# Performance work log

Hardware: AMD Instinct MI355X
Metric: run time of the kernel (lower is better)

## Reference

```python
import jax, jax.numpy as jnp
import numpy as np

N_NODES = 100_000
N_EDGES = 20_000   # hyperedges
NNZ = 2_000_000    # incidence pairs
F = 128
BN_EPS = 1e-5


def setup_inputs() -> dict:
    key = jax.random.key(0)
    ks = jax.random.split(key, 6)
    x_0 = jax.random.normal(ks[0], (N_NODES, F), dtype=jnp.float32)
    x_1 = jax.random.normal(ks[1], (N_EDGES, F), dtype=jnp.float32)
    node_idx = jax.random.randint(ks[2], (NNZ,), 0, N_NODES, dtype=jnp.int32)
    edge_idx = jax.random.randint(ks[3], (NNZ,), 0, N_EDGES, dtype=jnp.int32)
    W_nh = jax.random.normal(ks[4], (F, F), dtype=jnp.float32) / np.float32(np.sqrt(F))
    b_nh = jnp.zeros((F,), jnp.float32)
    W_en = jax.random.normal(ks[5], (F, 2 * F), dtype=jnp.float32) / np.float32(np.sqrt(2 * F))
    b_en = jnp.zeros((F,), jnp.float32)
    ones = jnp.ones((F,), jnp.float32)
    zeros = jnp.zeros((F,), jnp.float32)
    return {
        "x_0": x_0, "x_1": x_1, "node_idx": node_idx, "edge_idx": edge_idx,
        "W_nh": W_nh, "b_nh": b_nh, "W_en": W_en, "b_en": b_en,
        "bn0_gamma": ones, "bn0_beta": zeros, "bn0_mean": zeros, "bn0_var": ones,
        "bn1_gamma": ones, "bn1_beta": zeros, "bn1_mean": zeros, "bn1_var": ones,
    }


def _bn_eval(x, gamma, beta, mean, var):
    # BatchNorm1d in eval mode: normalize with running stats.
    return (x - mean) * (gamma * jax.lax.rsqrt(var + BN_EPS)) + beta


def reference(x_0, x_1, node_idx, edge_idx, W_nh, b_nh, W_en, b_en,
              bn0_gamma, bn0_beta, bn0_mean, bn0_var,
              bn1_gamma, bn1_beta, bn1_mean, bn1_var):
    # --- node -> hyperedge messenger ---
    # per-node message: sigmoid(Linear(x_0))  [n_nodes, F]
    node_messages = jax.nn.sigmoid(x_0 @ W_nh.T + b_nh)
    # gather over incidence list, scatter-sum onto hyperedges  [n_edges, F]
    node_msg_agg = jax.ops.segment_sum(node_messages[node_idx], edge_idx,
                                       num_segments=N_EDGES)

    # --- hyperedge -> node messenger ---
    # per-hyperedge message: sigmoid(Linear(cat(x_1, agg node msgs)))  [n_edges, F]
    he_messages = jax.nn.sigmoid(
        jnp.concatenate([x_1, node_msg_agg], axis=1) @ W_en.T + b_en)
    # gather per incidence, scatter-sum onto nodes  [n_nodes, F]
    he_msg_agg = jax.ops.segment_sum(he_messages[edge_idx], node_idx,
                                     num_segments=N_NODES)

    # --- updates (eval mode: feature dropout is identity) ---
    x0_out = jax.nn.sigmoid(
        _bn_eval(x_0, bn0_gamma, bn0_beta, bn0_mean, bn0_var) + he_msg_agg)
    x1_out = jax.nn.sigmoid(
        _bn_eval(x_1, bn1_gamma, bn1_beta, bn1_mean, bn1_var) + node_msg_agg)
    return (x0_out, x1_out)
```

## Files before the change

kernel.cpp:

```cpp
#include <hip/hip_runtime.h>
#include <hip/hip_bf16.h>
#include <math.h>

#define NNODES 100000
#define NEDGES 20000
#define NNZ_   2000000
#define FDIM   128
#define BN_EPS 1e-5f

#define NBUCK 256
#define CAP   9216
#define BPB_E 79
#define BPB_N 391
#define SH_E  17
#define SH_N  15

typedef __attribute__((ext_vector_type(8))) short bf16x8_t;
typedef __attribute__((ext_vector_type(4))) float f32x4_t;
typedef __attribute__((ext_vector_type(8))) unsigned short u16x8_t;

__device__ __forceinline__ float sigmoidf_(float x) {
    return 1.0f / (1.0f + __expf(-x));
}
__device__ __forceinline__ float bf2f(unsigned short u) {
    return __uint_as_float(((unsigned)u) << 16);
}
__device__ __forceinline__ unsigned short f2bf(float f) {
    __hip_bfloat16 h = __float2bfloat16(f);
    return *reinterpret_cast<unsigned short*>(&h);
}

__global__ __launch_bounds__(256) void prep_w(
    const float* __restrict__ W_nh, const float* __restrict__ W_en,
    unsigned short* __restrict__ Wnh_bf,
    unsigned short* __restrict__ W1hi, unsigned short* __restrict__ W1lo,
    unsigned short* __restrict__ W2hi, unsigned short* __restrict__ W2lo)
{
    int idx = blockIdx.x * blockDim.x + threadIdx.x;
    if (idx < FDIM * FDIM) {
        Wnh_bf[idx] = f2bf(W_nh[idx]);
        return;
    }
    int j = idx - FDIM * FDIM;
    if (j >= 2 * FDIM * FDIM) return;
    int n = j >> 8, kk = j & 255;
    float w = W_en[n * 2 * FDIM + kk];
    unsigned short hi = f2bf(w);
    unsigned short lo = f2bf(w - bf2f(hi));
    int o = n * FDIM + (kk & 127);
    if (kk < FDIM) { W1hi[o] = hi; W1lo[o] = lo; }
    else           { W2hi[o] = hi; W2lo[o] = lo; }
}

__global__ __launch_bounds__(256) void gemm1_mfma(
    const float* __restrict__ x0, const unsigned short* __restrict__ Wb,
    const float* __restrict__ bias, unsigned short* __restrict__ out)
{
    __shared__ unsigned short As[32][FDIM + 8];
    const int tid  = threadIdx.x;
    const int row0 = blockIdx.x * 32;
    {
        int r = tid >> 3, c0 = (tid & 7) * 16;
        const float* src = x0 + (size_t)(row0 + r) * FDIM + c0;
        unsigned short* dst = &As[r][c0];
        #pragma unroll
        for (int i = 0; i < 4; i++) {
            float4 v = *(const float4*)(src + i * 4);
            dst[i * 4 + 0] = f2bf(v.x);
            dst[i * 4 + 1] = f2bf(v.y);
            dst[i * 4 + 2] = f2bf(v.z);
            dst[i * 4 + 3] = f2bf(v.w);
        }
    }
    __syncthreads();
    const int wave  = tid >> 6;
    const int lane  = tid & 63;
    const int mhalf = wave & 1;
    const int nhalf = wave >> 1;
    const int lm    = lane & 15;
    const int quad  = lane >> 4;
    f32x4_t acc[4] = {};
    #pragma unroll
    for (int ks = 0; ks < 4; ks++) {
        bf16x8_t a = *(const bf16x8_t*)&As[mhalf * 16 + lm][ks * 32 + quad * 8];
        #pragma unroll
        for (int nt = 0; nt < 4; nt++) {
            int n = nhalf * 64 + nt * 16 + lm;
            bf16x8_t b = *(const bf16x8_t*)(Wb + (size_t)n * FDIM + ks * 32 + quad * 8);
            acc[nt] = __builtin_amdgcn_mfma_f32_16x16x32_bf16(a, b, acc[nt], 0, 0, 0);
        }
    }
    const int mbase = row0 + mhalf * 16 + quad * 4;
    #pragma unroll
    for (int nt = 0; nt < 4; nt++) {
        int n = nhalf * 64 + nt * 16 + lm;
        float bv = bias[n];
        #pragma unroll
        for (int r2 = 0; r2 < 4; r2++) {
            out[(size_t)(mbase + r2) * FDIM + n] = f2bf(sigmoidf_(acc[nt][r2] + bv));
        }
    }
}

__global__ __launch_bounds__(256) void gemm2_mfma(
    const float* __restrict__ x1, const float* __restrict__ Bagg,
    const unsigned short* __restrict__ W1hi, const unsigned short* __restrict__ W1lo,
    const unsigned short* __restrict__ W2hi, const unsigned short* __restrict__ W2lo,
    const float* __restrict__ bias, unsigned short* __restrict__ out)
{
    __shared__ unsigned short Ax[2][32][FDIM + 8];
    __shared__ unsigned short Ab[2][32][FDIM + 8];
    const int tid  = threadIdx.x;
    const int row0 = blockIdx.x * 32;
    {
        int r = tid >> 3, c0 = (tid & 7) * 16;
        const float* sx = x1   + (size_t)(row0 + r) * FDIM + c0;
        const float* sb = Bagg + (size_t)(row0 + r) * FDIM + c0;
        #pragma unroll
        for (int i = 0; i < 4; i++) {
            float4 v = *(const float4*)(sx + i * 4);
            float4 w = *(const float4*)(sb + i * 4);
            #pragma unroll
            for (int c = 0; c < 4; c++) {
                float fv = (c == 0) ? v.x : (c == 1) ? v.y : (c == 2) ? v.z : v.w;
                unsigned short h = f2bf(fv);
                Ax[0][r][c0 + i * 4 + c] = h;
                Ax[1][r][c0 + i * 4 + c] = f2bf(fv - bf2f(h));
                float fw = (c == 0) ? w.x : (c == 1) ? w.y : (c == 2) ? w.z : w.w;
                unsigned short hb = f2bf(fw);
                Ab[0][r][c0 + i * 4 + c] = hb;
                Ab[1][r][c0 + i * 4 + c] = f2bf(fw - bf2f(hb));
            }
        }
    }
    __syncthreads();
    const int wave  = tid >> 6;
    const int lane  = tid & 63;
    const int mhalf = wave & 1;
    const int nhalf = wave >> 1;
    const int lm    = lane & 15;
    const int quad  = lane >> 4;
    f32x4_t acc[4] = {};
    const unsigned short* Wsel[6] = {W1hi, W1hi, W1lo, W2hi, W2hi, W2lo};
    #pragma unroll
    for (int ps = 0; ps < 6; ps++) {
        const unsigned short (*Asel)[FDIM + 8] =
            (ps < 3) ? ((ps == 1) ? Ax[1] : Ax[0])
                     : ((ps == 4) ? Ab[1] : Ab[0]);
        const unsigned short* Wp = Wsel[ps];
        #pragma unroll
        for (int ks = 0; ks < 4; ks++) {
            bf16x8_t a = *(const bf16x8_t*)&Asel[mhalf * 16 + lm][ks * 32 + quad * 8];
            #pragma unroll
            for (int nt = 0; nt < 4; nt++) {
                int n = nhalf * 64 + nt * 16 + lm;
                bf16x8_t b = *(const bf16x8_t*)(Wp + (size_t)n * FDIM + ks * 32 + quad * 8);
                acc[nt] = __builtin_amdgcn_mfma_f32_16x16x32_bf16(a, b, acc[nt], 0, 0, 0);
            }
        }
    }
    const int mbase = row0 + mhalf * 16 + quad * 4;
    #pragma unroll
    for (int nt = 0; nt < 4; nt++) {
        int n = nhalf * 64 + nt * 16 + lm;
        float bv = bias[n];
        #pragma unroll
        for (int r2 = 0; r2 < 4; r2++) {
            out[(size_t)(mbase + r2) * FDIM + n] = f2bf(sigmoidf_(acc[nt][r2] + bv));
        }
    }
}

__global__ __launch_bounds__(1024) void bucket_scatter(
    const int* __restrict__ ni, const int* __restrict__ ei,
    unsigned* __restrict__ buck_e, unsigned* __restrict__ buck_n,
    int* __restrict__ gcur_e, int* __restrict__ gcur_n)
{
    __shared__ int lh_e[NBUCK], lh_n[NBUCK], lb_e[NBUCK], lb_n[NBUCK];
    const int t = threadIdx.x;
    if (t < NBUCK) { lh_e[t] = 0; lh_n[t] = 0; }
    __syncthreads();
    unsigned ent_e[4], ent_n[4];
    int be[4], bn[4], re[4], rn[4];
    const int base = blockIdx.x * 4096;
    #pragma unroll
    for (int j = 0; j < 4; j++) {
        int i = base + j * 1024 + t;
        if (i < NNZ_) {
            unsigned n = (unsigned)ni[i], e = (unsigned)ei[i];
            ent_e[j] = (e << SH_E) | n;  be[j] = (int)(e / BPB_E);
            ent_n[j] = (n << SH_N) | e;  bn[j] = (int)(n / BPB_N);
            re[j] = atomicAdd(&lh_e[be[j]], 1);
            rn[j] = atomicAdd(&lh_n[bn[j]], 1);
        } else { be[j] = -1; }
    }
    __syncthreads();
    if (t < NBUCK) {
        lb_e[t] = t * CAP + atomicAdd(&gcur_e[t], lh_e[t]);
        lb_n[t] = t * CAP + atomicAdd(&gcur_n[t], lh_n[t]);
    }
    __syncthreads();
    #pragma unroll
    for (int j = 0; j < 4; j++) {
        if (be[j] >= 0) {
            buck_e[(size_t)lb_e[be[j]] + re[j]] = ent_e[j];
            buck_n[(size_t)lb_n[bn[j]] + rn[j]] = ent_n[j];
        }
    }
}

template<int BPB, int SH, unsigned MASK, int NBINS, typename OUT>
__device__ __forceinline__ void sort_bucket(
    const unsigned* __restrict__ region, int cnt, int gbase, int b0,
    OUT* __restrict__ csr, int* __restrict__ off)
{
    __shared__ unsigned lh[512];
    __shared__ unsigned lw[4];
    const int t = threadIdx.x;
    lh[t] = 0; lh[t + 256] = 0;
    __syncthreads();
    for (int i = t; i < cnt; i += 256) {
        int bin = (int)(region[i] >> SH) - b0;
        atomicAdd(&lh[bin], 1u);
    }
    __syncthreads();
    unsigned h0 = lh[2 * t], h1 = lh[2 * t + 1];
    unsigned s = h0 + h1, inc = s;
    const int lane = t & 63;
    #pragma unroll
    for (int d = 1; d <= 32; d <<= 1) {
        unsigned v = (unsigned)__shfl_up((int)inc, d, 64);
        if (lane >= d) inc += v;
    }
    if (lane == 63) lw[t >> 6] = inc;
    __syncthreads();
    unsigned pre = 0;
    #pragma unroll
    for (int w = 0; w < 4; w++) if (w < (t >> 6)) pre += lw[w];
    unsigned excl = pre + inc - s;
    unsigned c0 = (unsigned)gbase + excl;
    unsigned c1 = c0 + h0;
    lh[2 * t] = c0; lh[2 * t + 1] = c1;
    int i0 = 2 * t, i1 = 2 * t + 1;
    if (i0 <= BPB && b0 + i0 <= NBINS) off[b0 + i0] = (int)c0;
    if (i1 <= BPB && b0 + i1 <= NBINS) off[b0 + i1] = (int)c1;
    __syncthreads();
    for (int i = t; i < cnt; i += 256) {
        unsigned ent = region[i];
        int bin = (int)(ent >> SH) - b0;
        unsigned pos = atomicAdd(&lh[bin], 1u);
        csr[pos] = (OUT)(ent & MASK);
    }
}

__global__ __launch_bounds__(256) void bucket_sort(
    const unsigned* __restrict__ buck_e, const unsigned* __restrict__ buck_n,
    const int* __restrict__ gcur_e, const int* __restrict__ gcur_n,
    unsigned* __restrict__ csr_e, unsigned short* __restrict__ csr_n,
    int* __restrict__ off_e, int* __restrict__ off_n)
{
    const int b = blockIdx.x & 255;
    const int* gc = (blockIdx.x < 256) ? gcur_e : gcur_n;
    __shared__ int ws4[4];
    const int t = threadIdx.x;
    int v = (t < b) ? gc[t] : 0;
    #pragma unroll
    for (int d = 32; d > 0; d >>= 1) v += __shfl_down(v, d, 64);
    if ((t & 63) == 0) ws4[t >> 6] = v;
    __syncthreads();
    const int gbase = ws4[0] + ws4[1] + ws4[2] + ws4[3];
    const int cnt = gc[b];
    __syncthreads();
    if (blockIdx.x < 256)
        sort_bucket<BPB_E, SH_E, 0x1FFFFu, NEDGES, unsigned>(
            buck_e + (size_t)b * CAP, cnt, gbase, b * BPB_E, csr_e, off_e);
    else
        sort_bucket<BPB_N, SH_N, 0x7FFFu, NNODES, unsigned short>(
            buck_n + (size_t)b * CAP, cnt, gbase, b * BPB_N, csr_n, off_n);
}

template<typename IDX, int U>
__global__ __launch_bounds__(256) void seg_sum_fin_v2(
    const unsigned short* __restrict__ table, const IDX* __restrict__ csr,
    const int* __restrict__ off, const float* __restrict__ x,
    const float* __restrict__ g, const float* __restrict__ bb,
    const float* __restrict__ mm, const float* __restrict__ vv,
    float* __restrict__ agg_out, float* __restrict__ fin_out, int nseg)
{
    const int seg = blockIdx.x * 4 + (threadIdx.x >> 6);
    if (seg >= nseg) return;
    const int lane = threadIdx.x & 63;
    const int c    = lane & 15;
    const int sub  = lane >> 4;
    const int c8   = c * 8;

    const int i0 = off[seg], i1 = off[seg + 1];
    f32x4_t a0 = {}, a1 = {};

    int i = i0;
    for (; i + 4 * U <= i1; i += 4 * U) {
        int r[U];
        u16x8_t v[U];
        #pragma unroll
        for (int u = 0; u < U; u++) r[u] = (int)csr[i + 4 * u + sub];
        #pragma unroll
        for (int u = 0; u < U; u++)
            v[u] = *(const u16x8_t*)(table + (size_t)r[u] * FDIM + c8);
        #pragma unroll
        for (int u = 0; u < U; u++) {
            a0[0] += bf2f(v[u][0]); a0[1] += bf2f(v[u][1]);
            a0[2] += bf2f(v[u][2]); a0[3] += bf2f(v[u][3]);
            a1[0] += bf2f(v[u][4]); a1[1] += bf2f(v[u][5]);
            a1[2] += bf2f(v[u][6]); a1[3] += bf2f(v[u][7]);
        }
    }
    if (i < i1) {
        u16x8_t v[U];
        #pragma unroll
        for (int u = 0; u < U; u++) {
            int row = i + 4 * u + sub;
            u16x8_t z = {};
            v[u] = z;
            if (row < i1)
                v[u] = *(const u16x8_t*)(table + (size_t)csr[row] * FDIM + c8);
        }
        #pragma unroll
        for (int u = 0; u < U; u++) {
            a0[0] += bf2f(v[u][0]); a0[1] += bf2f(v[u][1]);
            a0[2] += bf2f(v[u][2]); a0[3] += bf2f(v[u][3]);
            a1[0] += bf2f(v[u][4]); a1[1] += bf2f(v[u][5]);
            a1[2] += bf2f(v[u][6]); a1[3] += bf2f(v[u][7]);
        }
    }

    #pragma unroll
    for (int j = 0; j < 4; j++) {
        a0[j] += __shfl_xor(a0[j], 16, 64);
        a0[j] += __shfl_xor(a0[j], 32, 64);
        a1[j] += __shfl_xor(a1[j], 16, 64);
        a1[j] += __shfl_xor(a1[j], 32, 64);
    }

    if (sub < 2) {
        const int q = c8 + sub * 4;
        f32x4_t s = sub ? a1 : a0;
        if (agg_out)
            *(f32x4_t*)(agg_out + (size_t)seg * FDIM + q) = s;
        if (fin_out) {
            f32x4_t xv = *(const f32x4_t*)(x + (size_t)seg * FDIM + q);
            f32x4_t gg = *(const f32x4_t*)(g + q);
            f32x4_t bt = *(const f32x4_t*)(bb + q);
            f32x4_t mn = *(const f32x4_t*)(mm + q);
            f32x4_t vr = *(const f32x4_t*)(vv + q);
            f32x4_t o;
            #pragma unroll
            for (int j = 0; j < 4; j++)
                o[j] = sigmoidf_((xv[j] - mn[j]) * (gg[j] * rsqrtf(vr[j] + BN_EPS))
                                 + bt[j] + s[j]);
            *(f32x4_t*)(fin_out + (size_t)seg * FDIM + q) = o;
        }
    }
}

extern "C" void kernel_launch(void* const* d_in, const int* in_sizes, int n_in,
                              void* d_out, int out_size, void* d_ws, size_t ws_size,
                              hipStream_t stream)
{
    const float* x0       = (const float*)d_in[0];
    const float* x1       = (const float*)d_in[1];
    const int*   node_idx = (const int*)d_in[2];
    const int*   edge_idx = (const int*)d_in[3];
    const float* W_nh     = (const float*)d_in[4];
    const float* b_nh     = (const float*)d_in[5];
    const float* W_en     = (const float*)d_in[6];
    const float* b_en     = (const float*)d_in[7];
    const float* bn0g = (const float*)d_in[8];
    const float* bn0b = (const float*)d_in[9];
    const float* bn0m = (const float*)d_in[10];
    const float* bn0v = (const float*)d_in[11];
    const float* bn1g = (const float*)d_in[12];
    const float* bn1b = (const float*)d_in[13];
    const float* bn1m = (const float*)d_in[14];
    const float* bn1v = (const float*)d_in[15];

    float* ws = (float*)d_ws;
    float* B = ws;
    unsigned short* Wnh_bf = (unsigned short*)(B + (size_t)NEDGES * FDIM);
    unsigned short* W1hi = Wnh_bf + FDIM * FDIM;
    unsigned short* W1lo = W1hi + FDIM * FDIM;
    unsigned short* W2hi = W1lo + FDIM * FDIM;
    unsigned short* W2lo = W2hi + FDIM * FDIM;
    unsigned short* A_bf = W2lo + FDIM * FDIM;
    unsigned short* D_bf = A_bf + (size_t)NNODES * FDIM;
    int* off_e = (int*)(D_bf + (size_t)NEDGES * FDIM);
    int* off_n = off_e + 20004;
    unsigned* csr_e = (unsigned*)(off_n + 100004);
    unsigned short* csr_n = (unsigned short*)(csr_e + NNZ_);
    unsigned* buck_e = (unsigned*)(csr_n + NNZ_);
    unsigned* buck_n = buck_e + (size_t)NBUCK * CAP;
    int* gcur_e = (int*)(buck_n + (size_t)NBUCK * CAP);
    int* gcur_n = gcur_e + NBUCK;

    hipMemsetAsync(gcur_e, 0, 2 * NBUCK * sizeof(int), stream);
    bucket_scatter<<<(NNZ_ + 4095) / 4096, 1024, 0, stream>>>(
        node_idx, edge_idx, buck_e, buck_n, gcur_e, gcur_n);
    bucket_sort<<<2 * NBUCK, 256, 0, stream>>>(buck_e, buck_n, gcur_e, gcur_n,
                                               csr_e, csr_n, off_e, off_n);

    prep_w<<<(3 * FDIM * FDIM + 255) / 256, 256, 0, stream>>>(
        W_nh, W_en, Wnh_bf, W1hi, W1lo, W2hi, W2lo);

    float* out0 = (float*)d_out;
    float* out1 = out0 + (size_t)NNODES * FDIM;

    gemm1_mfma<<<NNODES / 32, 256, 0, stream>>>(x0, Wnh_bf, b_nh, A_bf);
    seg_sum_fin_v2<unsigned, 8><<<(NEDGES + 3) / 4, 256, 0, stream>>>(
        A_bf, csr_e, off_e, x1, bn1g, bn1b, bn1m, bn1v, B, out1, NEDGES);

    gemm2_mfma<<<NEDGES / 32, 256, 0, stream>>>(
        x1, B, W1hi, W1lo, W2hi, W2lo, b_en, D_bf);
    seg_sum_fin_v2<unsigned short, 4><<<(NNODES + 3) / 4, 256, 0, stream>>>(
        D_bf, csr_n, off_n, x0, bn0g, bn0b, bn0m, bn0v, nullptr, out0, NNODES);
}
```

Baseline: 384.9 us.

## Fuse bucket scatter with GEMM1, fold memset into prep, register-based GEMM2

Bucket scatter and the node GEMM now run as one launch: the leading blocks do the scatter and the rest run GEMM1 tiles. GEMM1 tiles load and convert A fragments straight into registers instead of staging them in shared memory. The gcur counters are zeroed inside prep_w, which replaces the separate memset and moves prep_w ahead of the fused kernel. GEMM2 also drops shared-memory staging, building hi/lo bf16 split fragments in registers and splitting columns across two blocks per row tile for more parallelism. This cuts launch count and LDS traffic, at the cost of redundant global loads and conversions of A across waves.

Result: slower. 393.8 us (+2.3%).

```diff
diff --git a/kernel.cpp b/kernel.cpp
--- a/kernel.cpp
+++ b/kernel.cpp
@@ -34,9 +34,11 @@
     const float* __restrict__ W_nh, const float* __restrict__ W_en,
     unsigned short* __restrict__ Wnh_bf,
     unsigned short* __restrict__ W1hi, unsigned short* __restrict__ W1lo,
-    unsigned short* __restrict__ W2hi, unsigned short* __restrict__ W2lo)
+    unsigned short* __restrict__ W2hi, unsigned short* __restrict__ W2lo,
+    int* __restrict__ gcur)
 {
     int idx = blockIdx.x * blockDim.x + threadIdx.x;
+    if (idx < 2 * NBUCK) gcur[idx] = 0;
     if (idx < FDIM * FDIM) {
         Wnh_bf[idx] = f2bf(W_nh[idx]);
         return;
@@ -52,41 +54,33 @@
     else           { W2hi[o] = hi; W2lo[o] = lo; }
 }
 
-__global__ __launch_bounds__(256) void gemm1_mfma(
+__device__ __forceinline__ void gemm1_tile(
     const float* __restrict__ x0, const unsigned short* __restrict__ Wb,
-    const float* __restrict__ bias, unsigned short* __restrict__ out)
-{
-    __shared__ unsigned short As[32][FDIM + 8];
-    const int tid  = threadIdx.x;
-    const int row0 = blockIdx.x * 32;
-    {
-        int r = tid >> 3, c0 = (tid & 7) * 16;
-        const float* src = x0 + (size_t)(row0 + r) * FDIM + c0;
-        unsigned short* dst = &As[r][c0];
-        #pragma unroll
-        for (int i = 0; i < 4; i++) {
-            float4 v = *(const float4*)(src + i * 4);
-            dst[i * 4 + 0] = f2bf(v.x);
-            dst[i * 4 + 1] = f2bf(v.y);
-            dst[i * 4 + 2] = f2bf(v.z);
-            dst[i * 4 + 3] = f2bf(v.w);
-        }
-    }
-    __syncthreads();
+    const float* __restrict__ bias, unsigned short* __restrict__ out,
+    int row0, int tid)
+{
     const int wave  = tid >> 6;
     const int lane  = tid & 63;
     const int mhalf = wave & 1;
     const int nhalf = wave >> 1;
     const int lm    = lane & 15;
     const int quad  = lane >> 4;
+    const float* ar = x0 + (size_t)(row0 + mhalf * 16 + lm) * FDIM;
     f32x4_t acc[4] = {};
     #pragma unroll
     for (int ks = 0; ks < 4; ks++) {
-        bf16x8_t a = *(const bf16x8_t*)&As[mhalf * 16 + lm][ks * 32 + quad * 8];
+        const int ko = ks * 32 + quad * 8;
+        float4 f0 = *(const float4*)(ar + ko);
+        float4 f1 = *(const float4*)(ar + ko + 4);
+        bf16x8_t a;
+        a[0] = (short)f2bf(f0.x); a[1] = (short)f2bf(f0.y);
+        a[2] = (short)f2bf(f0.z); a[3] = (short)f2bf(f0.w);
+        a[4] = (short)f2bf(f1.x); a[5] = (short)f2bf(f1.y);
+        a[6] = (short)f2bf(f1.z); a[7] = (short)f2bf(f1.w);
         #pragma unroll
         for (int nt = 0; nt < 4; nt++) {
             int n = nhalf * 64 + nt * 16 + lm;
-            bf16x8_t b = *(const bf16x8_t*)(Wb + (size_t)n * FDIM + ks * 32 + quad * 8);
+            bf16x8_t b = *(const bf16x8_t*)(Wb + (size_t)n * FDIM + ko);
             acc[nt] = __builtin_amdgcn_mfma_f32_16x16x32_bf16(a, b, acc[nt], 0, 0, 0);
         }
     }
@@ -102,109 +96,126 @@
     }
 }
 
-__global__ __launch_bounds__(256) void gemm2_mfma(
+__global__ __launch_bounds__(1024) void scatter_gemm1(
+    const int* __restrict__ ni, const int* __restrict__ ei,
+    unsigned* __restrict__ buck_e, unsigned* __restrict__ buck_n,
+    int* __restrict__ gcur_e, int* __restrict__ gcur_n,
+    const float* __restrict__ x0, const unsigned short* __restrict__ Wb,
+    const float* __restrict__ bias, unsigned short* __restrict__ A_bf,
+    int nscatter)
+{
+    if (blockIdx.x < nscatter) {
+        __shared__ int lh_e[NBUCK], lh_n[NBUCK], lb_e[NBUCK], lb_n[NBUCK];
+        const int t = threadIdx.x;
+        if (t < NBUCK) { lh_e[t] = 0; lh_n[t] = 0; }
+        __syncthreads();
+        unsigned ent_e[4], ent_n[4];
+        int be[4], bn[4], re[4], rn[4];
+        const int base = blockIdx.x * 4096;
+        #pragma unroll
+        for (int j = 0; j < 4; j++) {
+            int i = base + j * 1024 + t;
+            if (i < NNZ_) {
+                unsigned n = (unsigned)ni[i], e = (unsigned)ei[i];
+                ent_e[j] = (e << SH_E) | n;  be[j] = (int)(e / BPB_E);
+                ent_n[j] = (n << SH_N) | e;  bn[j] = (int)(n / BPB_N);
+                re[j] = atomicAdd(&lh_e[be[j]], 1);
+                rn[j] = atomicAdd(&lh_n[bn[j]], 1);
+            } else { be[j] = -1; }
+        }
+        __syncthreads();
+        if (t < NBUCK) {
+            lb_e[t] = t * CAP + atomicAdd(&gcur_e[t], lh_e[t]);
+            lb_n[t] = t * CAP + atomicAdd(&gcur_n[t], lh_n[t]);
+        }
+        __syncthreads();
+        #pragma unroll
+        for (int j = 0; j < 4; j++) {
+            if (be[j] >= 0) {
+                buck_e[(size_t)lb_e[be[j]] + re[j]] = ent_e[j];
+                buck_n[(size_t)lb_n[bn[j]] + rn[j]] = ent_n[j];
+            }
+        }
+    } else {
+        const int bid  = blockIdx.x - nscatter;
+        const int row0 = bid * 128 + (threadIdx.x >> 8) * 32;
+        if (row0 >= NNODES) return;
+        gemm1_tile(x0, Wb, bias, A_bf, row0, threadIdx.x & 255);
+    }
+}
+
+__device__ __forceinline__ void mfma_pass2(
+    const bf16x8_t af[4], const unsigned short* __restrict__ W,
+    int ncol, int lm, int quad, f32x4_t acc[2])
+{
+    #pragma unroll
+    for (int ks = 0; ks < 4; ks++) {
+        #pragma unroll
+        for (int nt = 0; nt < 2; nt++) {
+            int n = ncol + nt * 16 + lm;
+            bf16x8_t b = *(const bf16x8_t*)(W + (size_t)n * FDIM + ks * 32 + quad * 8);
+            acc[nt] = __builtin_amdgcn_mfma_f32_16x16x32_bf16(af[ks], b, acc[nt], 0, 0, 0);
+        }
+    }
+}
+
+__global__ __launch_bounds__(256) void gemm2_reg(
     const float* __restrict__ x1, const float* __restrict__ Bagg,
     const unsigned short* __restrict__ W1hi, const unsigned short* __restrict__ W1lo,
     const unsigned short* __restrict__ W2hi, const unsigned short* __restrict__ W2lo,
     const float* __restrict__ bias, unsigned short* __restrict__ out)
 {
-    __shared__ unsigned short Ax[2][32][FDIM + 8];
-    __shared__ unsigned short Ab[2][32][FDIM + 8];
+    const int row0 = (blockIdx.x >> 1) * 32;
+    const int col0 = (blockIdx.x & 1) * 64;
     const int tid  = threadIdx.x;
-    const int row0 = blockIdx.x * 32;
-    {
-        int r = tid >> 3, c0 = (tid & 7) * 16;
-        const float* sx = x1   + (size_t)(row0 + r) * FDIM + c0;
-        const float* sb = Bagg + (size_t)(row0 + r) * FDIM + c0;
-        #pragma unroll
-        for (int i = 0; i < 4; i++) {
-            float4 v = *(const float4*)(sx + i * 4);
-            float4 w = *(const float4*)(sb + i * 4);
-            #pragma unroll
-            for (int c = 0; c < 4; c++) {
-                float fv = (c == 0) ? v.x : (c == 1) ? v.y : (c == 2) ? v.z : v.w;
-                unsigned short h = f2bf(fv);
-                Ax[0][r][c0 + i * 4 + c] = h;
-                Ax[1][r][c0 + i * 4 + c] = f2bf(fv - bf2f(h));
-                float fw = (c == 0) ? w.x : (c == 1) ? w.y : (c == 2) ? w.z : w.w;
-                unsigned short hb = f2bf(fw);
-                Ab[0][r][c0 + i * 4 + c] = hb;
-                Ab[1][r][c0 + i * 4 + c] = f2bf(fw - bf2f(hb));
-            }
-        }
-    }
-    __syncthreads();
     const int wave  = tid >> 6;
     const int lane  = tid & 63;
     const int mhalf = wave & 1;
-    const int nhalf = wave >> 1;
+    const int npair = wave >> 1;
     const int lm    = lane & 15;
     const int quad  = lane >> 4;
-    f32x4_t acc[4] = {};
-    const unsigned short* Wsel[6] = {W1hi, W1hi, W1lo, W2hi, W2hi, W2lo};
-    #pragma unroll
-    for (int ps = 0; ps < 6; ps++) {
-        const unsigned short (*Asel)[FDIM + 8] =
-            (ps < 3) ? ((ps == 1) ? Ax[1] : Ax[0])
-                     : ((ps == 4) ? Ab[1] : Ab[0]);
-        const unsigned short* Wp = Wsel[ps];
-        #pragma unroll
-        for (int ks = 0; ks < 4; ks++) {
-            bf16x8_t a = *(const bf16x8_t*)&Asel[mhalf * 16 + lm][ks * 32 + quad * 8];
-            #pragma unroll
-            for (int nt = 0; nt < 4; nt++) {
-                int n = nhalf * 64 + nt * 16 + lm;
-                bf16x8_t b = *(const bf16x8_t*)(Wp + (size_t)n * FDIM + ks * 32 + quad * 8);
-                acc[nt] = __builtin_amdgcn_mfma_f32_16x16x32_bf16(a, b, acc[nt], 0, 0, 0);
-            }
-        }
-    }
+    const int rowA  = row0 + mhalf * 16 + lm;
+    const float* xr = x1   + (size_t)rowA * FDIM;
+    const float* br = Bagg + (size_t)rowA * FDIM;
+
+    bf16x8_t axh[4], axl[4], abh[4], abl[4];
+    #pragma unroll
+    for (int ks = 0; ks < 4; ks++) {
+        const int ko = ks * 32 + quad * 8;
+        float4 f0 = *(const float4*)(xr + ko);
+        float4 f1 = *(const float4*)(xr + ko + 4);
+        float4 g0 = *(const float4*)(br + ko);
+        float4 g1 = *(const float4*)(br + ko + 4);
+        float fx[8] = {f0.x, f0.y, f0.z, f0.w, f1.x, f1.y, f1.z, f1.w};
+        float fb[8] = {g0.x, g0.y, g0.z, g0.w, g1.x, g1.y, g1.z, g1.w};
+        #pragma unroll
+        for (int j = 0; j < 8; j++) {
+            unsigned short h = f2bf(fx[j]);
+            axh[ks][j] = (short)h;
+            axl[ks][j] = (short)f2bf(fx[j] - bf2f(h));
+            unsigned short hb = f2bf(fb[j]);
+            abh[ks][j] = (short)hb;
+            abl[ks][j] = (short)f2bf(fb[j] - bf2f(hb));
+        }
+    }
+
+    f32x4_t acc[2] = {};
+    const int ncol = col0 + npair * 32;
+    mfma_pass2(axh, W1hi, ncol, lm, quad, acc);
+    mfma_pass2(axl, W1hi, ncol, lm, quad, acc);
+    mfma_pass2(axh, W1lo, ncol, lm, quad, acc);
+    mfma_pass2(abh, W2hi, ncol, lm, quad, acc);
+    mfma_pass2(abl, W2hi, ncol, lm, quad, acc);
+    mfma_pass2(abh, W2lo, ncol, lm, quad, acc);
+
     const int mbase = row0 + mhalf * 16 + quad * 4;
     #pragma unroll
-    for (int nt = 0; nt < 4; nt++) {
-        int n = nhalf * 64 + nt * 16 + lm;
+    for (int nt = 0; nt < 2; nt++) {
+        int n = ncol + nt * 16 + lm;
         float bv = bias[n];
         #pragma unroll
         for (int r2 = 0; r2 < 4; r2++) {
             out[(size_t)(mbase + r2) * FDIM + n] = f2bf(sigmoidf_(acc[nt][r2] + bv));
-        }
-    }
-}
-
-__global__ __launch_bounds__(1024) void bucket_scatter(
-    const int* __restrict__ ni, const int* __restrict__ ei,
-    unsigned* __restrict__ buck_e, unsigned* __restrict__ buck_n,
-    int* __restrict__ gcur_e, int* __restrict__ gcur_n)
-{
-    __shared__ int lh_e[NBUCK], lh_n[NBUCK], lb_e[NBUCK], lb_n[NBUCK];
-    const int t = threadIdx.x;
-    if (t < NBUCK) { lh_e[t] = 0; lh_n[t] = 0; }
-    __syncthreads();
-    unsigned ent_e[4], ent_n[4];
-    int be[4], bn[4], re[4], rn[4];
-    const int base = blockIdx.x * 4096;
-    #pragma unroll
-    for (int j = 0; j < 4; j++) {
-        int i = base + j * 1024 + t;
-        if (i < NNZ_) {
-            unsigned n = (unsigned)ni[i], e = (unsigned)ei[i];
-            ent_e[j] = (e << SH_E) | n;  be[j] = (int)(e / BPB_E);
-            ent_n[j] = (n << SH_N) | e;  bn[j] = (int)(n / BPB_N);
-            re[j] = atomicAdd(&lh_e[be[j]], 1);
-            rn[j] = atomicAdd(&lh_n[bn[j]], 1);
-        } else { be[j] = -1; }
-    }
-    __syncthreads();
-    if (t < NBUCK) {
-        lb_e[t] = t * CAP + atomicAdd(&gcur_e[t], lh_e[t]);
-        lb_n[t] = t * CAP + atomicAdd(&gcur_n[t], lh_n[t]);
-    }
-    __syncthreads();
-    #pragma unroll
-    for (int j = 0; j < 4; j++) {
-        if (be[j] >= 0) {
-            buck_e[(size_t)lb_e[be[j]] + re[j]] = ent_e[j];
-            buck_n[(size_t)lb_n[bn[j]] + rn[j]] = ent_n[j];
         }
     }
 }
@@ -401,24 +412,27 @@
     int* gcur_e = (int*)(buck_n + (size_t)NBUCK * CAP);
     int* gcur_n = gcur_e + NBUCK;
 
-    hipMemsetAsync(gcur_e, 0, 2 * NBUCK * sizeof(int), stream);
-    bucket_scatter<<<(NNZ_ + 4095) / 4096, 1024, 0, stream>>>(
-        node_idx, edge_idx, buck_e, buck_n, gcur_e, gcur_n);
+    prep_w<<<(3 * FDIM * FDIM + 255) / 256, 256, 0, stream>>>(
+        W_nh, W_en, Wnh_bf, W1hi, W1lo, W2hi, W2lo, gcur_e);
+
+    float* out0 = (float*)d_out;
+    float* out1 = out0 + (size_t)NNODES * FDIM;
+
+    const int nscatter = (NNZ_ + 4095) / 4096;
+    const int ngemm1   = (NNODES + 127) / 128;
+    scatter_gemm1<<<nscatter + ngemm1, 1024, 0, stream>>>(
+        node_idx, edge_idx, buck_e, buck_n, gcur_e, gcur_n,
+        x0, Wnh_bf, b_nh, A_bf, nscatter);
+
     bucket_sort<<<2 * NBUCK, 256, 0, stream>>>(buck_e, buck_n, gcur_e, gcur_n,
                                                csr_e, csr_n, off_e, off_n);
 
-    prep_w<<<(3 * FDIM * FDIM + 255) / 256, 256, 0, stream>>>(
-        W_nh, W_en, Wnh_bf, W1hi, W1lo, W2hi, W2lo);
-
-    float* out0 = (float*)d_out;
-    float* out1 = out0 + (size_t)NNODES * FDIM;
-
-    gemm1_mfma<<<NNODES / 32, 256, 0, stream>>>(x0, Wnh_bf, b_nh, A_bf);
     seg_sum_fin_v2<unsigned, 8><<<(NEDGES + 3) / 4, 256, 0, stream>>>(
         A_bf, csr_e, off_e, x1, bn1g, bn1b, bn1m, bn1v, B, out1, NEDGES);
 
-    gemm2_mfma<<<NEDGES / 32, 256, 0, stream>>>(
+    gemm2_reg<<<(NEDGES / 32) * 2, 256, 0, stream>>>(
         x1, B, W1hi, W1lo, W2hi, W2lo, b_en, D_bf);
+
     seg_sum_fin_v2<unsigned short, 4><<<(NNODES + 3) / 4, 256, 0, stream>>>(
         D_bf, csr_n, off_n, x0, bn0g, bn0b, bn0m, bn0v, nullptr, out0, NNODES);
 }
```
